# Optimization experiments

Hardware: AMD Instinct MI355X
Metric: run time of the kernel (lower is better)

## Reference

```python
import jax, jax.numpy as jnp
import numpy as np

B = 1024
NQ = 14
NL = 4


def _apply_single(psi_t, gate, q):
    # psi_t: (B, 2, ..., 2) with NQ qubit axes; gate: (2,2) or (B,2,2) complex64
    psi_m = jnp.moveaxis(psi_t, q + 1, -1)
    if gate.ndim == 3:
        new = jnp.einsum('b...i,bji->b...j', psi_m, gate)
    else:
        new = jnp.einsum('b...i,ji->b...j', psi_m, gate)
    return jnp.moveaxis(new, -1, q + 1)


def _apply_cnot(psi_t, c, t):
    # CNOT(control=c, target=t): flip target amplitudes on the control=1 slice
    ca, ta = c + 1, t + 1
    c0 = jax.lax.index_in_dim(psi_t, 0, ca, keepdims=False)
    c1 = jax.lax.index_in_dim(psi_t, 1, ca, keepdims=False)
    ta2 = ta - 1 if ta > ca else ta  # target axis shifts after control axis removal
    c1 = jnp.flip(c1, axis=ta2)  # X on target
    return jnp.stack([c0, c1], axis=ca)


def _forward(inputs, weights):
    Bn, nq = inputs.shape
    nl = weights.shape[0]
    dim = 2 ** nq
    # |0...0> initial state
    psi = jnp.zeros((Bn, dim), dtype=jnp.complex64).at[:, 0].set(1.0)
    psi = psi.reshape((Bn,) + (2,) * nq)
    # RY(theta) per-sample encoding gates: (B, nq, 2, 2)
    c = jnp.cos(inputs / 2).astype(jnp.complex64)
    s = jnp.sin(inputs / 2).astype(jnp.complex64)
    ry = jnp.stack([jnp.stack([c, -s], -1), jnp.stack([s, c], -1)], -2)
    # RX(theta) variational gates: (nl, nq, 2, 2)
    cw = jnp.cos(weights / 2).astype(jnp.complex64)
    sw = jnp.sin(weights / 2).astype(jnp.complex64)
    rx = jnp.stack([jnp.stack([cw, -1j * sw], -1), jnp.stack([-1j * sw, cw], -1)], -2)
    # Encoding layer
    for i in range(nq):
        psi = _apply_single(psi, ry[:, i], i)
    # Variational layers: CNOT chain then RX on every qubit
    for layer in range(nl):
        for i in range(nq - 1):
            psi = _apply_cnot(psi, i, i + 1)
        for i in range(nq):
            psi = _apply_single(psi, rx[layer, i], i)
    # Pauli-Z expectation per qubit
    probs = psi.real ** 2 + psi.imag ** 2  # (B, 2, ..., 2) float32
    exps = []
    for i in range(nq):
        p = jnp.moveaxis(probs, i + 1, 1).reshape(Bn, 2, -1).sum(-1)
        exps.append(p[:, 0] - p[:, 1])
    return jnp.stack(exps, axis=1).astype(jnp.float32)


def setup_inputs() -> dict:
    key = jax.random.key(0)
    k1, k2 = jax.random.split(key)
    inputs = jax.random.normal(k1, (B, NQ), dtype=jnp.float32)
    weights = 0.1 * jax.random.normal(k2, (NL, NQ), dtype=jnp.float32)
    return {"inputs": inputs, "weights": weights}


def reference(inputs, weights):
    return _forward(inputs, weights)
```

## Files before the change

### kernel.cpp

```cpp
#include <hip/hip_runtime.h>
#include <hip/hip_fp16.h>


typedef float v2f __attribute__((ext_vector_type(2)));

constexpr int NQ  = 14;
constexpr int DIM = 1 << NQ;
constexpr int NT  = 512;
constexpr int APT = DIM / NT;
constexpr int NL  = 4;

#define RXREG(QBIT, ANGLE)                                              \
    {                                                                   \
        float s_, c_;                                                   \
        __sincosf(0.5f * (ANGLE), &s_, &c_);                            \
        v2f sp; sp.x = s_; sp.y = -s_;                                  \
        _Pragma("unroll")                                               \
        for (int o = 0; o < APT; ++o) {                                 \
            if (o & (1 << (QBIT))) continue;                            \
            const int o1 = o | (1 << (QBIT));                           \
            v2f w0 = a[o1].yx, w1 = a[o].yx;                            \
            a[o]  = __builtin_elementwise_fma(sp, w0, c_ * a[o]);       \
            a[o1] = __builtin_elementwise_fma(sp, w1, c_ * a[o1]);      \
        }                                                               \
    }

#define SWEEP(WADDR, RADDR)                                             \
    {                                                                   \
        __half2* buf = lds + pb * DIM;                                  \
        _Pragma("unroll")                                               \
        for (int o = 0; o < APT; ++o)                                   \
            buf[WADDR] = __floats2half2_rn(a[o].x, a[o].y);             \
        __syncthreads();                                                \
        _Pragma("unroll")                                               \
        for (int o = 0; o < APT; ++o) {                                 \
            float2 f_ = __half22float2(buf[RADDR]);                     \
            a[o].x = f_.x; a[o].y = f_.y;                               \
        }                                                               \
        pb ^= 1;                                                        \
    }

__global__ __launch_bounds__(NT, 1)
void vqc_kernel(const float* __restrict__ inputs,
                const float* __restrict__ weights,
                float* __restrict__ out)
{
    extern __shared__ __half2 lds[];
    const int t    = threadIdx.x;
    const int b    = blockIdx.x;
    const int lane = t & 63;
    const int wv   = t >> 6;

    const int C_L0 = (t << 5) | ((t >> 1) & 31);
    const int Tp   = ((t << 5) ^ (t << 6)) & (DIM - 1);
    const int C_PR = Tp ^ ((Tp >> 6) & 31);
    const int C_L2 = (((t >> 5) << 10) | (t & 31)) ^ (((t >> 5) & 1) << 4);
    const int C_L1 = t ^ ((t >> 6) & 7);

    v2f a[APT];

    {
        float cs[NQ], sn[NQ];
#pragma unroll
        for (int q = 0; q < NQ; ++q)
            __sincosf(0.5f * inputs[b * NQ + q], &sn[q], &cs[q]);

        const int jbase = t << 5;
        const int srchi = (jbase ^ (jbase << 1)) & (DIM - 1);
        float base = 1.0f;
#pragma unroll
        for (int q = 6; q < NQ; ++q)
            base *= ((srchi >> q) & 1) ? sn[q] : cs[q];
#pragma unroll
        for (int o = 0; o < APT; ++o) {
            int j   = jbase | o;
            int src = (j ^ (j << 1)) & (DIM - 1);
            float v = base;
#pragma unroll
            for (int q = 0; q < 6; ++q)
                v *= ((src >> q) & 1) ? sn[q] : cs[q];
            a[o].x = v;
            a[o].y = 0.0f;
        }
    }

    int pb = 0;

#pragma unroll 1
    for (int layer = 0; layer < NL; ++layer) {
        const float* wl = weights + layer * NQ;

        if (layer > 0) {
            SWEEP(C_L1 ^ ((o << 9) | ((o & 3) << 3)), C_PR ^ (o ^ (o << 1)));
        }

#pragma unroll
        for (int q = 0; q < 5; ++q) RXREG(q, wl[q]);

        SWEEP(C_L0 ^ o, C_L2 ^ ((o << 5) | (o >> 1)));

#pragma unroll
        for (int q = 0; q < 5; ++q) RXREG(q, wl[5 + q]);

        SWEEP(C_L2 ^ ((o << 5) | (o >> 1)), C_L1 ^ ((o << 9) | ((o & 3) << 3)));

#pragma unroll
        for (int q = 10; q < NQ; ++q) RXREG(q - 9, wl[q]);
    }

    float ptot = 0.0f, Sq[5] = {0, 0, 0, 0, 0};
#pragma unroll
    for (int o = 0; o < APT; ++o) {
        float p = a[o].x * a[o].x + a[o].y * a[o].y;
        ptot += p;
#pragma unroll
        for (int m = 0; m < 5; ++m)
            Sq[m] += ((o >> m) & 1) ? -p : p;
    }

    float accL[6];
#pragma unroll
    for (int k = 0; k < 6; ++k) accL[k] = ptot;
#pragma unroll
    for (int k = 0; k < 6; ++k) {
        const int m = 1 << k;
#pragma unroll
        for (int j = 0; j < 6; ++j) {
            float pr = __shfl_xor(accL[j], m, 64);
            if (j == k)
                accL[j] = ((lane >> k) & 1) ? (pr - accL[j]) : (accL[j] - pr);
            else
                accL[j] += pr;
        }
        ptot += __shfl_xor(ptot, m, 64);
#pragma unroll
        for (int j = 0; j < 5; ++j) Sq[j] += __shfl_xor(Sq[j], m, 64);
    }

    float* red = reinterpret_cast<float*>(lds + DIM);
    if (lane == 0) {
        red[wv * 12 + 0] = ptot;
#pragma unroll
        for (int k = 0; k < 6; ++k) red[wv * 12 + 1 + k] = accL[k];
#pragma unroll
        for (int m = 0; m < 5; ++m) red[wv * 12 + 7 + m] = Sq[m];
    }
    __syncthreads();

    if (t < NQ) {
        float acc = 0.0f;
        if (t < 6) {
            for (int w = 0; w < 8; ++w) acc += red[w * 12 + 1 + t];
        } else if (t < 9) {
            const int bit = t - 6;
            for (int w = 0; w < 8; ++w) {
                float v = red[w * 12];
                acc += ((w >> bit) & 1) ? -v : v;
            }
        } else {
            for (int w = 0; w < 8; ++w) acc += red[w * 12 + 7 + (t - 9)];
        }
        out[b * NQ + t] = acc;
    }
}

extern "C" void kernel_launch(void* const* d_in, const int* in_sizes, int n_in,
                              void* d_out, int out_size, void* d_ws, size_t ws_size,
                              hipStream_t stream)
{
    const float* inputs  = (const float*)d_in[0];
    const float* weights = (const float*)d_in[1];
    float* out = (float*)d_out;

    const int Bn = in_sizes[0] / NQ;
    vqc_kernel<<<dim3(Bn), dim3(NT), 2 * DIM * sizeof(__half2), stream>>>(inputs, weights, out);
}
```

Before: 114.1 us.

## Process two samples per block with fp16 packed math, DPP butterflies and interleaved sweeps

After: 108.8 us. 1.05x faster.

```diff
diff --git a/kernel.cpp b/kernel.cpp
--- a/kernel.cpp
+++ b/kernel.cpp
@@ -2,7 +2,7 @@
 #include <hip/hip_fp16.h>
 
 
-typedef float v2f __attribute__((ext_vector_type(2)));
+typedef unsigned int u32;
 
 constexpr int NQ  = 14;
 constexpr int DIM = 1 << NQ;
@@ -10,37 +10,97 @@
 constexpr int APT = DIM / NT;
 constexpr int NL  = 4;
 
-#define RXREG(QBIT, ANGLE)                                              \
-    {                                                                   \
-        float s_, c_;                                                   \
-        __sincosf(0.5f * (ANGLE), &s_, &c_);                            \
-        v2f sp; sp.x = s_; sp.y = -s_;                                  \
-        _Pragma("unroll")                                               \
-        for (int o = 0; o < APT; ++o) {                                 \
-            if (o & (1 << (QBIT))) continue;                            \
-            const int o1 = o | (1 << (QBIT));                           \
-            v2f w0 = a[o1].yx, w1 = a[o].yx;                            \
-            a[o]  = __builtin_elementwise_fma(sp, w0, c_ * a[o]);       \
-            a[o1] = __builtin_elementwise_fma(sp, w1, c_ * a[o1]);      \
-        }                                                               \
-    }
+#define H2U(v) __builtin_bit_cast(u32, v)
+#define U2H(v) __builtin_bit_cast(__half2, v)
+#define DPP1(v) U2H((u32)__builtin_amdgcn_mov_dpp((int)H2U(v), 0xB1, 0xF, 0xF, true))
+#define DPP2(v) U2H((u32)__builtin_amdgcn_mov_dpp((int)H2U(v), 0x4E, 0xF, 0xF, true))
 
-#define SWEEP(WADDR, RADDR)                                             \
-    {                                                                   \
-        __half2* buf = lds + pb * DIM;                                  \
-        _Pragma("unroll")                                               \
-        for (int o = 0; o < APT; ++o)                                   \
-            buf[WADDR] = __floats2half2_rn(a[o].x, a[o].y);             \
-        __syncthreads();                                                \
-        _Pragma("unroll")                                               \
-        for (int o = 0; o < APT; ++o) {                                 \
-            float2 f_ = __half22float2(buf[RADDR]);                     \
-            a[o].x = f_.x; a[o].y = f_.y;                               \
-        }                                                               \
-        pb ^= 1;                                                        \
-    }
+#define TB(k) ((t >> (k)) & 1)
+#define TM(k) ((Tm >> (k)) & 1)
 
-__global__ __launch_bounds__(NT, 1)
+#define LOADSC(L, Q) { float2 sc_ = wtab[(L) * NQ + (Q)];               \
+    sp_ = __floats2half2_rn(sc_.x, -sc_.x);                             \
+    cc_ = __float2half2_rn(sc_.y); }
+
+#define RXBIT(ARR, BIT) { _Pragma("unroll")                             \
+    for (int o = 0; o < APT; ++o) {                                     \
+        if (o & (1 << (BIT))) continue;                                 \
+        const int o1_ = o | (1 << (BIT));                               \
+        __half2 t0_ = ARR[o], t1_ = ARR[o1_];                           \
+        ARR[o]   = __hfma2(sp_, __lowhigh2highlow(t1_), __hmul2(cc_, t0_)); \
+        ARR[o1_] = __hfma2(sp_, __lowhigh2highlow(t0_), __hmul2(cc_, t1_)); } }
+
+#define RXD(ARR, DPPM) { _Pragma("unroll")                              \
+    for (int o = 0; o < APT; ++o) {                                     \
+        __half2 p_ = DPPM(ARR[o]);                                      \
+        ARR[o] = __hfma2(sp_, __lowhigh2highlow(p_), __hmul2(cc_, ARR[o])); } }
+
+#define RXLOW(ARR, L)  { __half2 sp_, cc_;                              \
+    LOADSC(L,0)  RXBIT(ARR,0) LOADSC(L,1)  RXBIT(ARR,1)                 \
+    LOADSC(L,2)  RXBIT(ARR,2) LOADSC(L,3)  RXBIT(ARR,3)                 \
+    LOADSC(L,4)  RXBIT(ARR,4) LOADSC(L,5)  RXD(ARR,DPP1)                \
+    LOADSC(L,6)  RXD(ARR,DPP2) }
+#define RXHIGH(ARR, L) { __half2 sp_, cc_;                              \
+    LOADSC(L,7)  RXBIT(ARR,0) LOADSC(L,8)  RXBIT(ARR,1)                 \
+    LOADSC(L,9)  RXBIT(ARR,2) LOADSC(L,10) RXBIT(ARR,3)                 \
+    LOADSC(L,11) RXBIT(ARR,4) LOADSC(L,12) RXD(ARR,DPP1)                \
+    LOADSC(L,13) RXD(ARR,DPP2) }
+
+#define WS1(ARR, BUF) { uint2* b2_ = reinterpret_cast<uint2*>(BUF);     \
+    _Pragma("unroll") for (int o = 0; o < APT; o += 2)                  \
+        b2_[(CW1 ^ (o | (((o >> 1) & 15) << 10))) >> 1] =               \
+            make_uint2(H2U(ARR[o]), H2U(ARR[o + 1])); }
+#define RS1(ARR, BUF) { _Pragma("unroll") for (int o = 0; o < APT; ++o) \
+        ARR[o] = (BUF)[CR1 ^ (((o & 1) << 3) | (((o >> 1) & 15) << 4))]; }
+#define WS2(ARR, BUF) { uint2* b2_ = reinterpret_cast<uint2*>(BUF);     \
+    _Pragma("unroll") for (int o = 0; o < APT; o += 2)                  \
+        b2_[(CW2 ^ ((o & 15) | (((o >> 4) & 1) << 8) | (((o >> 1) & 7) << 10))) >> 1] = \
+            make_uint2(H2U(ARR[o]), H2U(ARR[o + 1])); }
+#define RS2(ARR, BUF) { _Pragma("unroll") for (int o = 0; o < APT; ++o) { \
+        const int op_ = (o ^ (o << 1)) & 63;                            \
+        ARR[o] = (BUF)[CR2 ^ (op_ << 1)]; } }
+
+#define ENCODE(ARR, ROW) {                                              \
+    float cs_[NQ], sn_[NQ];                                             \
+    _Pragma("unroll") for (int q = 0; q < NQ; ++q)                      \
+        __sincosf(0.5f * (ROW)[q], &sn_[q], &cs_[q]);                   \
+    float base_ = 1.0f;                                                 \
+    _Pragma("unroll") for (int q = 6; q < NQ; ++q)                      \
+        base_ *= ((Tm >> (q - 5)) & 1) ? sn_[q] : cs_[q];               \
+    _Pragma("unroll") for (int o = 0; o < APT; ++o) {                   \
+        const int op_ = o ^ (o << 1);                                   \
+        float v_ = base_;                                               \
+        _Pragma("unroll") for (int q = 0; q < 5; ++q)                   \
+            v_ *= ((op_ >> q) & 1) ? sn_[q] : cs_[q];                   \
+        v_ *= (((op_ >> 5) ^ t) & 1) ? sn_[5] : cs_[5];                 \
+        ARR[o] = __floats2half2_rn(v_, 0.0f); } }
+
+#define EXPECT(ARR, RED) {                                              \
+    float ptot = 0.f, Sq[5] = {0, 0, 0, 0, 0};                          \
+    _Pragma("unroll") for (int o = 0; o < APT; ++o) {                   \
+        float2 f_ = __half22float2(ARR[o]);                             \
+        float p_ = f_.x * f_.x + f_.y * f_.y;                           \
+        ptot += p_;                                                     \
+        _Pragma("unroll") for (int m = 0; m < 5; ++m)                   \
+            Sq[m] += ((o >> m) & 1) ? -p_ : p_; }                       \
+    float accL[6];                                                      \
+    _Pragma("unroll") for (int k = 0; k < 6; ++k) accL[k] = ptot;       \
+    _Pragma("unroll") for (int k = 0; k < 6; ++k) {                     \
+        const int m_ = 1 << k;                                          \
+        _Pragma("unroll") for (int j = 0; j < 6; ++j) {                 \
+            float pr_ = __shfl_xor(accL[j], m_, 64);                    \
+            if (j == k) accL[j] = ((lane >> k) & 1) ? (pr_ - accL[j])   \
+                                                    : (accL[j] - pr_);  \
+            else accL[j] += pr_; }                                      \
+        ptot += __shfl_xor(ptot, m_, 64);                               \
+        _Pragma("unroll") for (int j2 = 0; j2 < 5; ++j2)                \
+            Sq[j2] += __shfl_xor(Sq[j2], m_, 64); }                     \
+    if (lane == 0) {                                                    \
+        (RED)[wv * 12 + 0] = ptot;                                      \
+        _Pragma("unroll") for (int k = 0; k < 6; ++k) (RED)[wv * 12 + 1 + k] = accL[k]; \
+        _Pragma("unroll") for (int m2 = 0; m2 < 5; ++m2) (RED)[wv * 12 + 7 + m2] = Sq[m2]; } }
+
+__global__ __launch_bounds__(NT, 2)
 void vqc_kernel(const float* __restrict__ inputs,
                 const float* __restrict__ weights,
                 float* __restrict__ out)
@@ -50,117 +110,71 @@
     const int b    = blockIdx.x;
     const int lane = t & 63;
     const int wv   = t >> 6;
+    const int sA   = 2 * b, sB = 2 * b + 1;
+    const int Tm   = (t ^ (t << 1)) & 0x3FF;
 
-    const int C_L0 = (t << 5) | ((t >> 1) & 31);
-    const int Tp   = ((t << 5) ^ (t << 6)) & (DIM - 1);
-    const int C_PR = Tp ^ ((Tp >> 6) & 31);
-    const int C_L2 = (((t >> 5) << 10) | (t & 31)) ^ (((t >> 5) & 1) << 4);
-    const int C_L1 = t ^ ((t >> 6) & 7);
+    __half2* buf0 = lds;
+    __half2* buf1 = lds + DIM;
+    float2*  wtab = reinterpret_cast<float2*>(lds + 2 * DIM);
+    float*   redA = reinterpret_cast<float*>(wtab + 56);
+    float*   redB = redA + 96;
 
-    v2f a[APT];
+    const int CW1 = ((t & 3) << 1) | ((TB(2) ^ TB(8)) << 3) | ((TB(3) ^ TB(7)) << 4)
+                  | (((t >> 4) & 7) << 5) | (((t >> 7) & 3) << 8);
+    const int CR1 = TB(2) | ((TB(3) ^ TB(7)) << 1) | ((TB(4) ^ TB(8)) << 2)
+                  | ((TB(5) ^ TB(1)) << 3) | ((TB(6) ^ TB(0)) << 4)
+                  | (TB(0) << 8) | (TB(1) << 9) | (TB(3) << 10) | (TB(4) << 11)
+                  | (TB(5) << 12) | (TB(6) << 13);
+    const int CW2 = (TB(2) << 1) | (TB(3) << 2) | (TB(4) << 3)
+                  | ((TB(5) ^ TB(8) ^ TB(0)) << 4) | (TB(6) << 5) | (TB(7) << 6)
+                  | (TB(8) << 7) | (TB(1) << 9) | (TB(0) << 13);
+    const int CR2 = TM(2) | (TM(3) << 1) | (TM(4) << 2) | (TM(5) << 3)
+                  | ((TM(1) ^ TM(7)) << 4) | (TM(0) << 6) | (TM(1) << 7)
+                  | (TM(6) << 8) | (TM(8) << 9) | (TM(3) << 10) | (TM(4) << 11)
+                  | (TM(5) << 12) | (TM(7) << 13);
 
-    {
-        float cs[NQ], sn[NQ];
-#pragma unroll
-        for (int q = 0; q < NQ; ++q)
-            __sincosf(0.5f * inputs[b * NQ + q], &sn[q], &cs[q]);
-
-        const int jbase = t << 5;
-        const int srchi = (jbase ^ (jbase << 1)) & (DIM - 1);
-        float base = 1.0f;
-#pragma unroll
-        for (int q = 6; q < NQ; ++q)
-            base *= ((srchi >> q) & 1) ? sn[q] : cs[q];
-#pragma unroll
-        for (int o = 0; o < APT; ++o) {
-            int j   = jbase | o;
-            int src = (j ^ (j << 1)) & (DIM - 1);
-            float v = base;
-#pragma unroll
-            for (int q = 0; q < 6; ++q)
-                v *= ((src >> q) & 1) ? sn[q] : cs[q];
-            a[o].x = v;
-            a[o].y = 0.0f;
-        }
+    if (t < NL * NQ) {
+        float s_, c_;
+        __sincosf(0.5f * weights[t], &s_, &c_);
+        wtab[t].x = s_; wtab[t].y = c_;
     }
 
-    int pb = 0;
+    __half2 aA[APT], aB[APT];
+    ENCODE(aA, inputs + sA * NQ);
+    ENCODE(aB, inputs + sB * NQ);
+    __syncthreads();
+
+    RXLOW(aA, 0);
+    WS1(aA, buf0);                  RXLOW(aB, 0);   __syncthreads();
+    RS1(aA, buf0); WS1(aB, buf1);   RXHIGH(aA, 0);  __syncthreads();
+    RS1(aB, buf1); WS2(aA, buf0);   RXHIGH(aB, 0);  __syncthreads();
 
 #pragma unroll 1
-    for (int layer = 0; layer < NL; ++layer) {
-        const float* wl = weights + layer * NQ;
-
-        if (layer > 0) {
-            SWEEP(C_L1 ^ ((o << 9) | ((o & 3) << 3)), C_PR ^ (o ^ (o << 1)));
-        }
-
-#pragma unroll
-        for (int q = 0; q < 5; ++q) RXREG(q, wl[q]);
-
-        SWEEP(C_L0 ^ o, C_L2 ^ ((o << 5) | (o >> 1)));
-
-#pragma unroll
-        for (int q = 0; q < 5; ++q) RXREG(q, wl[5 + q]);
-
-        SWEEP(C_L2 ^ ((o << 5) | (o >> 1)), C_L1 ^ ((o << 9) | ((o & 3) << 3)));
-
-#pragma unroll
-        for (int q = 10; q < NQ; ++q) RXREG(q - 9, wl[q]);
+    for (int l = 1; l < NL; ++l) {
+        RS2(aA, buf0); WS2(aB, buf1);  RXLOW(aA, l);   __syncthreads();
+        RS2(aB, buf1); WS1(aA, buf0);  RXLOW(aB, l);   __syncthreads();
+        RS1(aA, buf0); WS1(aB, buf1);  RXHIGH(aA, l);  __syncthreads();
+        RS1(aB, buf1); WS2(aA, buf0);  RXHIGH(aB, l);  __syncthreads();
     }
 
-    float ptot = 0.0f, Sq[5] = {0, 0, 0, 0, 0};
-#pragma unroll
-    for (int o = 0; o < APT; ++o) {
-        float p = a[o].x * a[o].x + a[o].y * a[o].y;
-        ptot += p;
-#pragma unroll
-        for (int m = 0; m < 5; ++m)
-            Sq[m] += ((o >> m) & 1) ? -p : p;
-    }
-
-    float accL[6];
-#pragma unroll
-    for (int k = 0; k < 6; ++k) accL[k] = ptot;
-#pragma unroll
-    for (int k = 0; k < 6; ++k) {
-        const int m = 1 << k;
-#pragma unroll
-        for (int j = 0; j < 6; ++j) {
-            float pr = __shfl_xor(accL[j], m, 64);
-            if (j == k)
-                accL[j] = ((lane >> k) & 1) ? (pr - accL[j]) : (accL[j] - pr);
-            else
-                accL[j] += pr;
-        }
-        ptot += __shfl_xor(ptot, m, 64);
-#pragma unroll
-        for (int j = 0; j < 5; ++j) Sq[j] += __shfl_xor(Sq[j], m, 64);
-    }
-
-    float* red = reinterpret_cast<float*>(lds + DIM);
-    if (lane == 0) {
-        red[wv * 12 + 0] = ptot;
-#pragma unroll
-        for (int k = 0; k < 6; ++k) red[wv * 12 + 1 + k] = accL[k];
-#pragma unroll
-        for (int m = 0; m < 5; ++m) red[wv * 12 + 7 + m] = Sq[m];
-    }
+    EXPECT(aA, redA);
+    EXPECT(aB, redB);
     __syncthreads();
 
     if (t < NQ) {
-        float acc = 0.0f;
-        if (t < 6) {
-            for (int w = 0; w < 8; ++w) acc += red[w * 12 + 1 + t];
-        } else if (t < 9) {
-            const int bit = t - 6;
-            for (int w = 0; w < 8; ++w) {
-                float v = red[w * 12];
-                acc += ((w >> bit) & 1) ? -v : v;
-            }
-        } else {
-            for (int w = 0; w < 8; ++w) acc += red[w * 12 + 7 + (t - 9)];
+        float accA = 0.f, accB = 0.f;
+#pragma unroll 1
+        for (int w = 0; w < 8; ++w) {
+            float vA, vB;
+            if (t < 4)       { vA = redA[w * 12 + 3 + t];        vB = redB[w * 12 + 3 + t]; }
+            else if (t < 7)  { vA = redA[w * 12];                vB = redB[w * 12];
+                               if ((w >> (t - 4)) & 1) { vA = -vA; vB = -vB; } }
+            else if (t < 12) { vA = redA[w * 12 + 7 + (t - 7)];  vB = redB[w * 12 + 7 + (t - 7)]; }
+            else             { vA = redA[w * 12 + 1 + (t - 12)]; vB = redB[w * 12 + 1 + (t - 12)]; }
+            accA += vA; accB += vB;
         }
-        out[b * NQ + t] = acc;
+        out[sA * NQ + t] = accA;
+        out[sB * NQ + t] = accB;
     }
 }
 
@@ -173,5 +187,6 @@
     float* out = (float*)d_out;
 
     const int Bn = in_sizes[0] / NQ;
-    vqc_kernel<<<dim3(Bn), dim3(NT), 2 * DIM * sizeof(__half2), stream>>>(inputs, weights, out);
+    const size_t shmem = 2 * DIM * sizeof(__half2) + 56 * sizeof(float2) + 192 * sizeof(float);
+    vqc_kernel<<<dim3(Bn / 2), dim3(NT), shmem, stream>>>(inputs, weights, out);
 }
```

## Keep state in packed half2 registers with 256 threads and wave-shuffle gates

Applied to the files above, without the earlier changes.

After: 106.7 us. 1.07x faster.

```diff
diff --git a/kernel.cpp b/kernel.cpp
--- a/kernel.cpp
+++ b/kernel.cpp
@@ -2,45 +2,65 @@
 #include <hip/hip_fp16.h>
 
 
-typedef float v2f __attribute__((ext_vector_type(2)));
+typedef unsigned int u32;
 
 constexpr int NQ  = 14;
 constexpr int DIM = 1 << NQ;
-constexpr int NT  = 512;
+constexpr int NT  = 256;
 constexpr int APT = DIM / NT;
 constexpr int NL  = 4;
 
-#define RXREG(QBIT, ANGLE)                                              \
-    {                                                                   \
-        float s_, c_;                                                   \
-        __sincosf(0.5f * (ANGLE), &s_, &c_);                            \
-        v2f sp; sp.x = s_; sp.y = -s_;                                  \
-        _Pragma("unroll")                                               \
-        for (int o = 0; o < APT; ++o) {                                 \
-            if (o & (1 << (QBIT))) continue;                            \
-            const int o1 = o | (1 << (QBIT));                           \
-            v2f w0 = a[o1].yx, w1 = a[o].yx;                            \
-            a[o]  = __builtin_elementwise_fma(sp, w0, c_ * a[o]);       \
-            a[o1] = __builtin_elementwise_fma(sp, w1, c_ * a[o1]);      \
-        }                                                               \
-    }
-
-#define SWEEP(WADDR, RADDR)                                             \
-    {                                                                   \
-        __half2* buf = lds + pb * DIM;                                  \
-        _Pragma("unroll")                                               \
-        for (int o = 0; o < APT; ++o)                                   \
-            buf[WADDR] = __floats2half2_rn(a[o].x, a[o].y);             \
-        __syncthreads();                                                \
-        _Pragma("unroll")                                               \
-        for (int o = 0; o < APT; ++o) {                                 \
-            float2 f_ = __half22float2(buf[RADDR]);                     \
-            a[o].x = f_.x; a[o].y = f_.y;                               \
-        }                                                               \
-        pb ^= 1;                                                        \
-    }
-
-__global__ __launch_bounds__(NT, 1)
+#define H2U(v) __builtin_bit_cast(u32, v)
+#define U2H(v) __builtin_bit_cast(__half2, v)
+
+#define PRELOAD(L, Q0, N) { _Pragma("unroll")                           \
+    for (int i_ = 0; i_ < (N); ++i_) {                                  \
+        uint2 w_ = wtab[(L) * NQ + (Q0) + i_];                          \
+        sw[i_] = __builtin_amdgcn_readfirstlane((int)w_.x);             \
+        cw[i_] = __builtin_amdgcn_readfirstlane((int)w_.y); } }
+
+#define RXQs(QBIT, I) {                                                 \
+    const __half2 sp_ = U2H((u32)sw[I]), cc_ = U2H((u32)cw[I]);         \
+    _Pragma("unroll")                                                   \
+    for (int o = 0; o < APT; ++o) {                                     \
+        if (o & (1 << (QBIT))) continue;                                \
+        const int o1_ = o | (1 << (QBIT));                              \
+        __half2 w0_ = __lowhigh2highlow(a[o1_]);                        \
+        __half2 w1_ = __lowhigh2highlow(a[o]);                          \
+        a[o]   = __hfma2(sp_, w0_, __hmul2(cc_, a[o]));                 \
+        a[o1_] = __hfma2(sp_, w1_, __hmul2(cc_, a[o1_])); } }
+
+#define RXS(MASK, I) {                                                  \
+    const __half2 sp_ = U2H((u32)sw[I]), cc_ = U2H((u32)cw[I]);         \
+    _Pragma("unroll")                                                   \
+    for (int o = 0; o < APT; ++o) {                                     \
+        int pi_ = __shfl_xor((int)H2U(a[o]), (MASK), 64);               \
+        __half2 p_ = __lowhigh2highlow(U2H((u32)pi_));                  \
+        a[o] = __hfma2(sp_, p_, __hmul2(cc_, a[o])); } }
+
+#define RXP0 { RXQs(0,0) RXQs(1,1) RXQs(2,2) RXQs(3,3) RXQs(4,4)        \
+               RXQs(5,5) RXS(1,6) RXS(2,7) }
+#define RXP1 { RXQs(0,0) RXQs(1,1) RXQs(2,2) RXQs(3,3) RXQs(4,4) RXQs(5,5) }
+
+#define OA1K(k) ((((k)&1)?0x82:0)^(((k)&2)?0x104:0)^(((k)&4)?0x208:0)   \
+               ^ (((k)&8)?0x410:0)^(((k)&16)?0x820:0))
+#define OA1R(o) ((((o)&15)<<3) | (((o)>>4)<<12))
+#define OB2K(k) ((((k)&1)?0x202:0)^(((k)&2)?0x404:0)^(((k)&4)?0x808:0)  \
+               ^ (((k)&8)?0x1010:0)^(((k)&16)?0x2000:0))
+#define OB2R(o) ((((o) ^ ((o)<<1)) & 0x7F) << 1)
+
+#define WS1 { _Pragma("unroll") for (int k = 0; k < 32; ++k)            \
+    *reinterpret_cast<uint2*>(buf + (CA1W ^ OA1K(k))) =                 \
+        make_uint2(H2U(a[2*k]), H2U(a[2*k+1])); }
+#define RS1 { _Pragma("unroll") for (int o = 0; o < APT; ++o)           \
+    a[o] = buf[CA1R ^ OA1R(o)]; }
+#define WS2 { _Pragma("unroll") for (int k = 0; k < 32; ++k)            \
+    *reinterpret_cast<uint2*>(buf + (CB2W ^ OB2K(k))) =                 \
+        make_uint2(H2U(a[2*k]), H2U(a[2*k+1])); }
+#define RS2 { _Pragma("unroll") for (int o = 0; o < APT; ++o)           \
+    a[o] = buf[CB2R ^ OB2R(o)]; }
+
+__global__ __launch_bounds__(NT, 2)
 void vqc_kernel(const float* __restrict__ inputs,
                 const float* __restrict__ weights,
                 float* __restrict__ out)
@@ -51,114 +71,131 @@
     const int lane = t & 63;
     const int wv   = t >> 6;
 
-    const int C_L0 = (t << 5) | ((t >> 1) & 31);
-    const int Tp   = ((t << 5) ^ (t << 6)) & (DIM - 1);
-    const int C_PR = Tp ^ ((Tp >> 6) & 31);
-    const int C_L2 = (((t >> 5) << 10) | (t & 31)) ^ (((t >> 5) & 1) << 4);
-    const int C_L1 = t ^ ((t >> 6) & 7);
-
-    v2f a[APT];
+    __half2* buf  = lds;
+    uint2*   wtab = reinterpret_cast<uint2*>(lds + DIM);
+    float2*  itab = reinterpret_cast<float2*>(wtab + 56);
+    float*   red  = reinterpret_cast<float*>(itab + 14);
+
+    const int t0 = t & 1, t1 = (t >> 1) & 1, t2 = (t >> 2) & 1, t3 = (t >> 3) & 1,
+              t4 = (t >> 4) & 1, t5 = (t >> 5) & 1, t6 = (t >> 6) & 1,
+              t7 = (t >> 7) & 1;
+
+    const int CA1W = ((t & 63) << 1) | ((t >> 6) << 12);
+    const int CA1R = (t0 ? 1 : 0) ^ (t1 ? 0x82 : 0) ^ (t2 ? 0x104 : 0)
+                   ^ (t3 ? 0x208 : 0) ^ (t4 ? 0x410 : 0) ^ (t5 ? 0x820 : 0)
+                   ^ (t6 ? 2 : 0) ^ (t7 ? 4 : 0);
+    const int CB2W = ((t & 63) << 1) | ((t >> 6) << 7);
+    const int s6 = t0, s7 = t1 ^ t0, s8 = t2 ^ t1, s9 = t3 ^ t2,
+              s10 = t4 ^ t3, s11 = t5 ^ t4, s12 = t6 ^ t5, s13 = t7 ^ t6;
+    const int CB2R = (s6 ? 0x80 : 0) ^ (s7 ? 0x100 : 0) ^ (s8 ? 1 : 0)
+                   ^ (s9 ? 0x202 : 0) ^ (s10 ? 0x404 : 0) ^ (s11 ? 0x808 : 0)
+                   ^ (s12 ? 0x1010 : 0) ^ (s13 ? 0x2000 : 0);
+
+    if (t < NL * NQ) {
+        float s_, c_;
+        __sincosf(0.5f * weights[t], &s_, &c_);
+        wtab[t] = make_uint2(H2U(__floats2half2_rn(s_, -s_)), H2U(__float2half2_rn(c_)));
+    }
+    if (t >= 64 && t < 64 + NQ) {
+        float s_, c_;
+        __sincosf(0.5f * inputs[b * NQ + (t - 64)], &s_, &c_);
+        itab[t - 64] = make_float2(s_, c_);
+    }
+    __syncthreads();
+
+    int sw[8], cw[8];
+    __half2 a[APT];
 
     {
-        float cs[NQ], sn[NQ];
-#pragma unroll
-        for (int q = 0; q < NQ; ++q)
-            __sincosf(0.5f * inputs[b * NQ + q], &sn[q], &cs[q]);
-
-        const int jbase = t << 5;
-        const int srchi = (jbase ^ (jbase << 1)) & (DIM - 1);
+        const int Tme = ((t << 6) ^ (t << 7)) & 0x3FFF;
         float base = 1.0f;
 #pragma unroll
-        for (int q = 6; q < NQ; ++q)
-            base *= ((srchi >> q) & 1) ? sn[q] : cs[q];
+        for (int q = 7; q < NQ; ++q) {
+            float2 f_ = itab[q];
+            base *= ((Tme >> q) & 1) ? f_.x : f_.y;
+        }
+        float2 f6 = itab[6];
+        float g6a = (t & 1) ? f6.x : f6.y;
+        float g6b = (t & 1) ? f6.y : f6.x;
+        float2 f0 = itab[0], f1 = itab[1], f2 = itab[2],
+               f3 = itab[3], f4 = itab[4], f5 = itab[5];
 #pragma unroll
         for (int o = 0; o < APT; ++o) {
-            int j   = jbase | o;
-            int src = (j ^ (j << 1)) & (DIM - 1);
-            float v = base;
-#pragma unroll
-            for (int q = 0; q < 6; ++q)
-                v *= ((src >> q) & 1) ? sn[q] : cs[q];
-            a[o].x = v;
-            a[o].y = 0.0f;
-        }
-    }
-
-    int pb = 0;
+            const int op = (o ^ (o << 1)) & 0x3F;
+            float v = base * ((o & 32) ? g6b : g6a);
+            v *= (op & 1)  ? f0.x : f0.y;
+            v *= (op & 2)  ? f1.x : f1.y;
+            v *= (op & 4)  ? f2.x : f2.y;
+            v *= (op & 8)  ? f3.x : f3.y;
+            v *= (op & 16) ? f4.x : f4.y;
+            v *= (op & 32) ? f5.x : f5.y;
+            a[o] = __floats2half2_rn(v, 0.0f);
+        }
+    }
+
+    PRELOAD(0, 0, 8);
+    RXP0;
+    WS1;  __syncthreads();  RS1;  __syncthreads();
+    PRELOAD(0, 8, 6);
+    RXP1;
 
 #pragma unroll 1
-    for (int layer = 0; layer < NL; ++layer) {
-        const float* wl = weights + layer * NQ;
-
-        if (layer > 0) {
-            SWEEP(C_L1 ^ ((o << 9) | ((o & 3) << 3)), C_PR ^ (o ^ (o << 1)));
-        }
-
-#pragma unroll
-        for (int q = 0; q < 5; ++q) RXREG(q, wl[q]);
-
-        SWEEP(C_L0 ^ o, C_L2 ^ ((o << 5) | (o >> 1)));
-
-#pragma unroll
-        for (int q = 0; q < 5; ++q) RXREG(q, wl[5 + q]);
-
-        SWEEP(C_L2 ^ ((o << 5) | (o >> 1)), C_L1 ^ ((o << 9) | ((o & 3) << 3)));
-
-#pragma unroll
-        for (int q = 10; q < NQ; ++q) RXREG(q - 9, wl[q]);
-    }
-
-    float ptot = 0.0f, Sq[5] = {0, 0, 0, 0, 0};
-#pragma unroll
-    for (int o = 0; o < APT; ++o) {
-        float p = a[o].x * a[o].x + a[o].y * a[o].y;
-        ptot += p;
-#pragma unroll
-        for (int m = 0; m < 5; ++m)
-            Sq[m] += ((o >> m) & 1) ? -p : p;
-    }
-
-    float accL[6];
-#pragma unroll
-    for (int k = 0; k < 6; ++k) accL[k] = ptot;
-#pragma unroll
-    for (int k = 0; k < 6; ++k) {
-        const int m = 1 << k;
-#pragma unroll
-        for (int j = 0; j < 6; ++j) {
-            float pr = __shfl_xor(accL[j], m, 64);
-            if (j == k)
-                accL[j] = ((lane >> k) & 1) ? (pr - accL[j]) : (accL[j] - pr);
-            else
-                accL[j] += pr;
-        }
-        ptot += __shfl_xor(ptot, m, 64);
-#pragma unroll
-        for (int j = 0; j < 5; ++j) Sq[j] += __shfl_xor(Sq[j], m, 64);
-    }
-
-    float* red = reinterpret_cast<float*>(lds + DIM);
-    if (lane == 0) {
-        red[wv * 12 + 0] = ptot;
-#pragma unroll
-        for (int k = 0; k < 6; ++k) red[wv * 12 + 1 + k] = accL[k];
-#pragma unroll
-        for (int m = 0; m < 5; ++m) red[wv * 12 + 7 + m] = Sq[m];
+    for (int l = 1; l < NL; ++l) {
+        WS2;  __syncthreads();  RS2;  __syncthreads();
+        PRELOAD(l, 0, 8);
+        RXP0;
+        WS1;  __syncthreads();  RS1;  __syncthreads();
+        PRELOAD(l, 8, 6);
+        RXP1;
+    }
+
+    {
+        float ptot = 0.f, Sq[6] = {0, 0, 0, 0, 0, 0};
+#pragma unroll
+        for (int o = 0; o < APT; ++o) {
+            float2 f_ = __half22float2(a[o]);
+            float p_ = f_.x * f_.x + f_.y * f_.y;
+            ptot += p_;
+#pragma unroll
+            for (int m = 0; m < 6; ++m)
+                Sq[m] += ((o >> m) & 1) ? -p_ : p_;
+        }
+        float accL[6];
+#pragma unroll
+        for (int k = 0; k < 6; ++k) accL[k] = ptot;
+#pragma unroll
+        for (int k = 0; k < 6; ++k) {
+            const int m_ = 1 << k;
+#pragma unroll
+            for (int j = 0; j < 6; ++j) {
+                float pr_ = __shfl_xor(accL[j], m_, 64);
+                if (j == k) accL[j] = ((lane >> k) & 1) ? (pr_ - accL[j]) : (accL[j] - pr_);
+                else        accL[j] += pr_;
+            }
+            ptot += __shfl_xor(ptot, m_, 64);
+#pragma unroll
+            for (int j2 = 0; j2 < 6; ++j2) Sq[j2] += __shfl_xor(Sq[j2], m_, 64);
+        }
+        if (lane == 0) {
+            red[wv * 13 + 0] = ptot;
+#pragma unroll
+            for (int k = 0; k < 6; ++k) red[wv * 13 + 1 + k] = accL[k];
+#pragma unroll
+            for (int m2 = 0; m2 < 6; ++m2) red[wv * 13 + 7 + m2] = Sq[m2];
+        }
     }
     __syncthreads();
 
     if (t < NQ) {
-        float acc = 0.0f;
-        if (t < 6) {
-            for (int w = 0; w < 8; ++w) acc += red[w * 12 + 1 + t];
-        } else if (t < 9) {
-            const int bit = t - 6;
-            for (int w = 0; w < 8; ++w) {
-                float v = red[w * 12];
-                acc += ((w >> bit) & 1) ? -v : v;
-            }
-        } else {
-            for (int w = 0; w < 8; ++w) acc += red[w * 12 + 7 + (t - 9)];
+        float acc = 0.f;
+#pragma unroll 1
+        for (int w = 0; w < 4; ++w) {
+            float v;
+            if (t < 6)       v = red[w * 13 + 1 + t];
+            else if (t == 6) { v = red[w * 13]; if (w & 1)        v = -v; }
+            else if (t == 7) { v = red[w * 13]; if ((w >> 1) & 1) v = -v; }
+            else             v = red[w * 13 + 7 + (t - 8)];
+            acc += v;
         }
         out[b * NQ + t] = acc;
     }
@@ -173,5 +210,8 @@
     float* out = (float*)d_out;
 
     const int Bn = in_sizes[0] / NQ;
-    vqc_kernel<<<dim3(Bn), dim3(NT), 2 * DIM * sizeof(__half2), stream>>>(inputs, weights, out);
+    const size_t shmem = DIM * sizeof(__half2)
+                       + 56 * sizeof(uint2) + 14 * sizeof(float2)
+                       + 52 * sizeof(float);
+    vqc_kernel<<<dim3(Bn), dim3(NT), shmem, stream>>>(inputs, weights, out);
 }
```
